# Optimization experiments

Hardware: AMD Instinct MI355X
Metric: run time of the kernel (lower is better)

The kernel has to match this reference:

```python
import jax, jax.numpy as jnp
import numpy as np

B, Hd, Wd, C, NH, WS = 8, 128, 128, 192, 6, 8
HDIM = int(C * 2.0)   # FFN hidden = 384
RED = C // 8          # AIM channel-gate reduction = 24


def setup_inputs() -> dict:
    key = jax.random.key(0)
    ks = jax.random.split(key, 12)
    s = 0.02
    return {
        "x": jax.random.normal(ks[0], (B, Hd * Wd, C), jnp.float32),
        "H": Hd,
        "W": Wd,
        "n1_w": jnp.ones((C,), jnp.float32),
        "n1_b": jnp.zeros((C,), jnp.float32),
        "qkv_w": jax.random.normal(ks[1], (C, 3 * C), jnp.float32) * s,
        "proj_w": jax.random.normal(ks[2], (C, C), jnp.float32) * s,
        "proj_b": jnp.zeros((C,), jnp.float32),
        "attn_bias": jax.random.normal(ks[3], (NH, WS * WS, WS * WS), jnp.float32) * s,
        "conv_w": jax.random.normal(ks[4], (C, 1, 3, 3), jnp.float32) * s,
        "cg_w1": jax.random.normal(ks[5], (RED, C), jnp.float32) * s,
        "cg_w2": jax.random.normal(ks[6], (C, RED), jnp.float32) * s,
        "n2_w": jnp.ones((C,), jnp.float32),
        "n2_b": jnp.zeros((C,), jnp.float32),
        "fc1_w": jax.random.normal(ks[7], (C, HDIM), jnp.float32) * s,
        "smix_w": jax.random.normal(ks[8], (HDIM, 1, 3, 3), jnp.float32) * s,
        "fc2_w": jax.random.normal(ks[9], (HDIM, C), jnp.float32) * s,
    }


def _ln(x, w, b):
    m = x.mean(-1, keepdims=True)
    v = ((x - m) ** 2).mean(-1, keepdims=True)
    return (x - m) * jax.lax.rsqrt(v + 1e-5) * w + b


def _dwconv(x, w, H, W):
    # x: [B, L, Cx] -> depthwise 3x3 'same' conv -> [B, L, Cx]
    Bx, L, Cx = x.shape
    xi = x.transpose(0, 2, 1).reshape(Bx, Cx, H, W)
    y = jax.lax.conv_general_dilated(
        xi, w, (1, 1), 'SAME', feature_group_count=Cx,
        dimension_numbers=('NCHW', 'OIHW', 'NCHW'))
    return y.reshape(Bx, Cx, L).transpose(0, 2, 1)


def _window_attn(x, H, W, qkv_w, proj_w, proj_b, bias):
    Bx, L, Cx = x.shape
    nHw, nWw = H // WS, W // WS  # H, W are multiples of WS here (no padding needed)
    hd = Cx // NH
    # [B, L, C] -> [B*nH*nW, ws*ws, C]
    xw = (x.reshape(Bx, nHw, WS, nWw, WS, Cx)
           .transpose(0, 1, 3, 2, 4, 5)
           .reshape(Bx * nHw * nWw, WS * WS, Cx))
    qkv = (xw @ qkv_w).reshape(-1, WS * WS, 3, NH, hd).transpose(2, 0, 3, 1, 4)
    q, k, v = qkv[0], qkv[1], qkv[2]          # [Bw, nh, N, hd]
    logits = (q * hd ** -0.5) @ k.transpose(0, 1, 3, 2) + bias[None]
    attn = jax.nn.softmax(logits, axis=-1)
    out = (attn @ v).transpose(0, 2, 1, 3).reshape(-1, WS * WS, Cx)
    out = out @ proj_w + proj_b
    # windows -> [B, L, C]
    return (out.reshape(Bx, nHw, nWw, WS, WS, Cx)
               .transpose(0, 1, 3, 2, 4, 5)
               .reshape(Bx, L, Cx))


def reference(x, H, W, n1_w, n1_b, qkv_w, proj_w, proj_b, attn_bias,
              conv_w, cg_w1, cg_w2, n2_w, n2_b, fc1_w, smix_w, fc2_w):
    n1 = _ln(x, n1_w, n1_b)
    attn_feat = _window_attn(n1, H, W, qkv_w, proj_w, proj_b, attn_bias)
    conv_feat = jax.nn.gelu(_dwconv(n1, conv_w, H, W), approximate=False)
    # AIM: channel_modulates_spatial (btype == 'spatial')
    pooled = conv_feat.mean(axis=1)                                   # [B, C]
    cm = jax.nn.sigmoid(jax.nn.gelu(pooled @ cg_w1.T, approximate=False) @ cg_w2.T)
    x = x + attn_feat * cm[:, None, :] + conv_feat                    # residual (DropPath=id)
    # FFN with depthwise spatial mixing
    n2 = _ln(x, n2_w, n2_b)
    h = jax.nn.gelu(n2 @ fc1_w, approximate=False)                    # [B, L, HDIM]
    h = _dwconv(h, smix_w, H, W)
    return x + h @ fc2_w
```

## Files before the change

### kernel.cpp

```cpp
#include <hip/hip_runtime.h>
#include <hip/hip_bf16.h>
#include <math.h>

#define BATCH 8
#define CCH 192
#define LTOK 16384
#define BL 131072LL
#define NWIN 2048
#define NHEADS 6

typedef __hip_bfloat16 bf16;
typedef __bf16 bfr;
typedef bfr bf16x8 __attribute__((ext_vector_type(8)));
typedef float f32x4 __attribute__((ext_vector_type(4)));
typedef unsigned short u16x8 __attribute__((ext_vector_type(8)));
typedef unsigned short u16x4 __attribute__((ext_vector_type(4)));
typedef unsigned int u32x2 __attribute__((ext_vector_type(2)));

#define FX     0
#define FN1W   1
#define FN1B   2
#define FQKVW  3
#define FPROJW 4
#define FPROJB 5
#define FBIAS  6
#define FCONVW 7
#define FCG1   8
#define FCG2   9
#define FN2W   10
#define FN2B   11
#define FFC1   12
#define FSMIX  13
#define FFC2   14

struct InPtrs { const void* p[15]; int n[15]; };

__device__ __forceinline__ float ldin(const void* p, long long i, int f32) {
    return f32 ? ((const float*)p)[i]
               : __bfloat162float(((const bf16*)p)[i]);
}

__device__ __forceinline__ float bfcvt(unsigned short u) {
    return __uint_as_float((unsigned)u << 16);
}

__device__ __forceinline__ f32x4 ld4f(const void* p, long long i, int f32) {
    if (f32) return *(const f32x4*)((const float*)p + i);
    u16x4 v = *(const u16x4*)((const bf16*)p + i);
    f32x4 r;
    r[0] = bfcvt(v[0]); r[1] = bfcvt(v[1]); r[2] = bfcvt(v[2]); r[3] = bfcvt(v[3]);
    return r;
}
__device__ __forceinline__ f32x4 ld4b(const bf16* p, long long i) {
    u16x4 v = *(const u16x4*)(p + i);
    f32x4 r;
    r[0] = bfcvt(v[0]); r[1] = bfcvt(v[1]); r[2] = bfcvt(v[2]); r[3] = bfcvt(v[3]);
    return r;
}
__device__ __forceinline__ void st4b(bf16* p, long long i, f32x4 v) {
    union { bf16 h; unsigned short u; } cv;
    u16x4 o;
    cv.h = __float2bfloat16(v[0]); o[0] = cv.u;
    cv.h = __float2bfloat16(v[1]); o[1] = cv.u;
    cv.h = __float2bfloat16(v[2]); o[2] = cv.u;
    cv.h = __float2bfloat16(v[3]); o[3] = cv.u;
    *(u16x4*)(p + i) = o;
}

__device__ __forceinline__ unsigned pk2bf(float a, float b) {
    union { bf16 h; unsigned short u; } ca, cb;
    ca.h = __float2bfloat16(a);
    cb.h = __float2bfloat16(b);
    return (unsigned)ca.u | ((unsigned)cb.u << 16);
}

__device__ __forceinline__ float gelu_f(float v) {
    return 0.5f * v * (1.0f + erff(v * 0.70710678118654752f));
}

__global__ void probe_k(InPtrs in, int* flags) {
    __shared__ int s_insane, s_evennz, s_oddnz;
    if (threadIdx.x == 0) { s_insane = 0; s_evennz = 0; s_oddnz = 0; }
    __syncthreads();
    int t = blockIdx.x;
    const bf16* p = (const bf16*)in.p[t];
    int n = in.n[t];
    int m = n < 2048 ? n : 2048;
    bool insane = false, evennz = false, oddnz = false;
    for (int i = threadIdx.x; i < m; i += 256) {
        float v = __bfloat162float(p[i]);
        if (!(fabsf(v) <= 1e9f)) insane = true;
        if (v != 0.0f) { if (i & 1) oddnz = true; else evennz = true; }
    }
    if (insane) s_insane = 1;
    if (evennz) s_evennz = 1;
    if (oddnz)  s_oddnz = 1;
    __syncthreads();
    if (threadIdx.x == 0)
        flags[t] = (s_insane || (!s_evennz && s_oddnz)) ? 1 : 0;
}

__global__ void transpose_k(const void* __restrict__ W, bf16* __restrict__ WT,
                            int K, int N, const int* flag) {
    int f = *flag;
    int idx = blockIdx.x * 256 + threadIdx.x;
    if (idx >= K * N) return;
    int k = idx / N, n = idx % N;
    WT[(long long)n * K + k] = __float2bfloat16(ldin(W, idx, f));
}

__global__ void convw_k(const void* __restrict__ W, float* __restrict__ WT,
                        int CX, const int* flag) {
    int f = *flag;
    int idx = blockIdx.x * 256 + threadIdx.x;
    if (idx >= CX * 9) return;
    int c = idx / 9, t = idx - c * 9;
    WT[t * CX + c] = ldin(W, idx, f);
}

__global__ __launch_bounds__(256)
void ln_kernel(const void* __restrict__ x, const void* __restrict__ w,
               const void* __restrict__ b, bf16* __restrict__ out,
               const int* flags) {
    int fx = flags[FX], fw = flags[FN1W], fb = flags[FN1B];
    int wv = threadIdx.x >> 6, lane = threadIdx.x & 63;
    int gw = lane >> 4, l16 = lane & 15;
    long long t = (long long)blockIdx.x * 16 + wv * 4 + gw;
    long long base = t * CCH;
    f32x4 v[3];
#pragma unroll
    for (int k = 0; k < 3; ++k)
        v[k] = ld4f(x, base + l16 * 4 + 64 * k, fx);
    float s = 0.f;
#pragma unroll
    for (int k = 0; k < 3; ++k) s += v[k][0] + v[k][1] + v[k][2] + v[k][3];
    s += __shfl_xor(s, 1); s += __shfl_xor(s, 2);
    s += __shfl_xor(s, 4); s += __shfl_xor(s, 8);
    float mean = s * (1.0f / 192.0f);
    float vs = 0.f;
#pragma unroll
    for (int k = 0; k < 3; ++k)
#pragma unroll
        for (int j = 0; j < 4; ++j) {
            float d = v[k][j] - mean;
            vs += d * d;
        }
    vs += __shfl_xor(vs, 1); vs += __shfl_xor(vs, 2);
    vs += __shfl_xor(vs, 4); vs += __shfl_xor(vs, 8);
    float rstd = rsqrtf(vs * (1.0f / 192.0f) + 1e-5f);
#pragma unroll
    for (int k = 0; k < 3; ++k) {
        int c0 = l16 * 4 + 64 * k;
        f32x4 wv4 = ld4f(w, c0, fw);
        f32x4 bv4 = ld4f(b, c0, fb);
        f32x4 o;
#pragma unroll
        for (int j = 0; j < 4; ++j)
            o[j] = (v[k][j] - mean) * rstd * wv4[j] + bv4[j];
        st4b(out, base + c0, o);
    }
}

template<int EPI, int KK, int NN, typename CT>
__global__ __launch_bounds__(256)
void gemm2_k(const bf16* __restrict__ A_, const bf16* __restrict__ BT_,
             CT* __restrict__ Cmat, const void* __restrict__ bias,
             const float* __restrict__ res, const int* __restrict__ flags) {
    constexpr int KT = KK / 192;
    constexpr int NC = NN / 64;
    constexpr int NITER = NC * KT;
    constexpr int GSTR = KK * 2;
    __shared__ __align__(16) char Ts[64 * 384];

    const int fb = (EPI == 1) ? flags[FPROJB] : 0;
    const int tid = threadIdx.x;
    const int lane = tid & 63, wv = tid >> 6;
    const int r16 = lane & 15, q = lane >> 4;
    const long long m0 = (long long)blockIdx.x * 64;
    const int swz = (r16 & 7) << 4;

    f32x4 pre[6];
    auto loadB = [&](int itn) {
        int nc2 = itn / KT, kt2 = itn - nc2 * KT;
#pragma unroll
        for (int p = 0; p < 6; ++p) {
            int off = p * 4096 + tid * 16;
            int row = off / 384, col = off - row * 384;
            pre[p] = *(const f32x4*)((const char*)BT_ +
                     (long long)(nc2 * 64 + row) * GSTR + kt2 * 384 + col);
        }
    };
    auto writeT = [&]() {
#pragma unroll
        for (int p = 0; p < 6; ++p) {
            int off = p * 4096 + tid * 16;
            int row = off / 384, col = off - row * 384;
            *(f32x4*)(Ts + row * 384 + (col ^ ((row & 7) << 4))) = pre[p];
        }
    };

    loadB(0);

    bf16x8 afrag[KK / 32];
    const char* Arow = Ts + (wv * 16 + r16) * 384;
    const char* asrc = (const char*)(A_ + m0 * KK);
#pragma unroll
    for (int kt = 0; kt < KT; ++kt) {
#pragma unroll
        for (int p = 0; p < 6; ++p) {
            int off = p * 4096 + tid * 16;
            int row = off / 384, col = off - row * 384;
            *(f32x4*)(Ts + row * 384 + (col ^ ((row & 7) << 4))) =
                *(const f32x4*)(asrc + (long long)row * GSTR + kt * 384 + col);
        }
        __syncthreads();
#pragma unroll
        for (int ks = 0; ks < 6; ++ks)
            afrag[kt * 6 + ks] = *(const bf16x8*)(Arow + ((ks * 64 + q * 16) ^ swz));
        __syncthreads();
    }
    writeT();
    __syncthreads();

    f32x4 acc0, acc1, acc2, acc3;
    float resv[16];

    for (int it = 0; it < NITER; ++it) {
        const int nc = it / KT, kt = it - nc * KT;
        if (kt == 0) {
            acc0 = f32x4{0.f, 0.f, 0.f, 0.f};
            acc1 = acc0; acc2 = acc0; acc3 = acc0;
            if (EPI == 3) {
#pragma unroll
                for (int j = 0; j < 4; ++j)
#pragma unroll
                    for (int r = 0; r < 4; ++r)
                        resv[j * 4 + r] =
                            res[(m0 + wv * 16 + q * 4 + r) * NN + nc * 64 + j * 16 + r16];
            }
        }
        const bool nxt = (it + 1 < NITER);
        if (nxt) loadB(it + 1);
#pragma unroll
        for (int ks = 0; ks < 6; ++ks) {
            bf16x8 a = afrag[kt * 6 + ks];
            const char* bb = Ts + r16 * 384 + ((ks * 64 + q * 16) ^ swz);
            bf16x8 b0 = *(const bf16x8*)(bb);
            bf16x8 b1 = *(const bf16x8*)(bb + 16 * 384);
            bf16x8 b2 = *(const bf16x8*)(bb + 32 * 384);
            bf16x8 b3 = *(const bf16x8*)(bb + 48 * 384);
            acc0 = __builtin_amdgcn_mfma_f32_16x16x32_bf16(a, b0, acc0, 0, 0, 0);
            acc1 = __builtin_amdgcn_mfma_f32_16x16x32_bf16(a, b1, acc1, 0, 0, 0);
            acc2 = __builtin_amdgcn_mfma_f32_16x16x32_bf16(a, b2, acc2, 0, 0, 0);
            acc3 = __builtin_amdgcn_mfma_f32_16x16x32_bf16(a, b3, acc3, 0, 0, 0);
        }
        __syncthreads();
        if (nxt) writeT();
        if (kt == KT - 1) {
            f32x4 accs[4] = {acc0, acc1, acc2, acc3};
#pragma unroll
            for (int j = 0; j < 4; ++j) {
                int col = nc * 64 + j * 16 + r16;
#pragma unroll
                for (int r = 0; r < 4; ++r) {
                    long long row = m0 + wv * 16 + q * 4 + r;
                    float v = accs[j][r];
                    if (EPI == 1) v += ldin(bias, col, fb);
                    if (EPI == 2) v = gelu_f(v);
                    if (EPI == 3) v += resv[j * 4 + r];
                    Cmat[row * NN + col] = (CT)v;
                }
            }
        }
        if (nxt) __syncthreads();
    }
}

__global__ __launch_bounds__(384)
void attn_proj_k(const bf16* __restrict__ qkv, const void* __restrict__ bias,
                 const bf16* __restrict__ pwT, const void* __restrict__ proj_b,
                 bf16* __restrict__ attnf, const int* __restrict__ flags) {
    __shared__ __align__(16) char SM[24576];

    const int fbias = flags[FBIAS];
    const int h = threadIdx.x >> 6, lane = threadIdx.x & 63;
    const int w = blockIdx.x;
    const int b = w >> 8, rem = w & 255, wy = rem >> 4, wx = rem & 15;
    const int l15 = lane & 15, quad = lane >> 4;
    const long long tokbase = (long long)b * LTOK + (wy * 8) * 128 + wx * 8;
    bfr* vtp = (bfr*)(SM + h * 4096);

    long long vt = tokbase + (lane >> 3) * 128 + (lane & 7);
    const bfr* vp = (const bfr*)(qkv + vt * 576 + 384 + h * 32);
    bf16x8 v0 = *(const bf16x8*)(vp);
    bf16x8 v1 = *(const bf16x8*)(vp + 8);
    bf16x8 v2 = *(const bf16x8*)(vp + 16);
    bf16x8 v3 = *(const bf16x8*)(vp + 24);

    bf16x8 aq[4], bk[4];
#pragma unroll
    for (int mt = 0; mt < 4; ++mt) {
        int i0 = mt * 16 + l15;
        long long t = tokbase + (i0 >> 3) * 128 + (i0 & 7);
        const bfr* qp = (const bfr*)(qkv + t * 576 + h * 32 + quad * 8);
        aq[mt] = *(const bf16x8*)qp;
        bk[mt] = *(const bf16x8*)(qp + 192);
    }

#pragma unroll
    for (int j = 0; j < 8; ++j) {
        int sc = lane ^ (j << 3);
        vtp[j * 64 + sc]        = v0[j];
        vtp[(j + 8) * 64 + sc]  = v1[j];
        vtp[(j + 16) * 64 + sc] = v2[j];
        vtp[(j + 24) * 64 + sc] = v3[j];
    }

    f32x4 T[4][4];
#pragma unroll
    for (int ti = 0; ti < 4; ++ti)
#pragma unroll
        for (int tj = 0; tj < 4; ++tj) {
            f32x4 z = {0.f, 0.f, 0.f, 0.f};
            T[ti][tj] = __builtin_amdgcn_mfma_f32_16x16x32_bf16(bk[ti], aq[tj], z, 0, 0, 0);
        }

    const float scale = 0.17677669529663689f;
    const long long bias0 = (long long)h * 4096;
    unsigned Wreg[4][4][2];
#pragma unroll
    for (int tj = 0; tj < 4; ++tj) {
        const long long brow = bias0 + (tj * 16 + l15) * 64 + quad * 4;
        float mloc = -3.0e38f;
#pragma unroll
        for (int ti = 0; ti < 4; ++ti) {
            f32x4 bv4 = ld4f(bias, brow + ti * 16, fbias);
#pragma unroll
            for (int r = 0; r < 4; ++r) {
                float v = T[ti][tj][r] * scale + bv4[r];
                T[ti][tj][r] = v;
                mloc = fmaxf(mloc, v);
            }
        }
        mloc = fmaxf(mloc, __shfl_xor(mloc, 16));
        mloc = fmaxf(mloc, __shfl_xor(mloc, 32));
        float l = 0.f;
#pragma unroll
        for (int ti = 0; ti < 4; ++ti)
#pragma unroll
            for (int r = 0; r < 4; ++r) {
                float e = __expf(T[ti][tj][r] - mloc);
                T[ti][tj][r] = e;
                l += e;
            }
        l += __shfl_xor(l, 16);
        l += __shfl_xor(l, 32);
        float linv = 1.0f / l;
#pragma unroll
        for (int ti = 0; ti < 4; ++ti) {
            Wreg[tj][ti][0] = pk2bf(T[ti][tj][0] * linv, T[ti][tj][1] * linv);
            Wreg[tj][ti][1] = pk2bf(T[ti][tj][2] * linv, T[ti][tj][3] * linv);
        }
    }

    const int vsw = (l15 & 7) << 3;
    bf16x8 bv[2][2];
#pragma unroll
    for (int kc = 0; kc < 2; ++kc) {
        bv[kc][0] = *(const bf16x8*)&vtp[l15 * 64 + ((kc * 32 + quad * 8) ^ vsw)];
        bv[kc][1] = *(const bf16x8*)&vtp[(16 + l15) * 64 + ((kc * 32 + quad * 8) ^ vsw)];
    }
    const int hi = quad >> 1, qlow = quad & 1;
    f32x4 O[4][2];
#pragma unroll
    for (int tj = 0; tj < 4; ++tj) {
        O[tj][0] = f32x4{0.f, 0.f, 0.f, 0.f};
        O[tj][1] = O[tj][0];
    }
#pragma unroll
    for (int tj = 0; tj < 4; ++tj)
#pragma unroll
        for (int kc = 0; kc < 2; ++kc) {
            union { unsigned u[4]; bf16x8 v; } ap;
#pragma unroll
            for (int j2 = 0; j2 < 4; ++j2) {
                int srcl = (2 * qlow + (j2 >> 1)) * 16 + l15;
                unsigned va = (unsigned)__shfl((int)Wreg[tj][2 * kc][j2 & 1], srcl);
                unsigned vb = (unsigned)__shfl((int)Wreg[tj][2 * kc + 1][j2 & 1], srcl);
                ap.u[j2] = hi ? vb : va;
            }
            O[tj][0] = __builtin_amdgcn_mfma_f32_16x16x32_bf16(ap.v, bv[kc][0], O[tj][0], 0, 0, 0);
            O[tj][1] = __builtin_amdgcn_mfma_f32_16x16x32_bf16(ap.v, bv[kc][1], O[tj][1], 0, 0, 0);
        }

    __syncthreads();

#pragma unroll
    for (int tj = 0; tj < 4; ++tj)
#pragma unroll
        for (int n2 = 0; n2 < 2; ++n2)
#pragma unroll
            for (int r = 0; r < 4; ++r) {
                int row = tj * 16 + quad * 4 + r;
                int cb = (h * 64 + n2 * 32 + l15 * 2) ^ ((row & 7) << 4);
                *(bf16*)(SM + row * 384 + cb) = __float2bfloat16(O[tj][n2][r]);
            }

    __syncthreads();

    const int fpb = flags[FPROJB];
    const int csw = (l15 & 7) << 4;
    f32x4 pacc[4][2];
#pragma unroll
    for (int mt = 0; mt < 4; ++mt) {
        pacc[mt][0] = f32x4{0.f, 0.f, 0.f, 0.f};
        pacc[mt][1] = pacc[mt][0];
    }
#pragma unroll
    for (int ks = 0; ks < 6; ++ks) {
        bf16x8 af[4];
#pragma unroll
        for (int mt = 0; mt < 4; ++mt)
            af[mt] = *(const bf16x8*)(SM + (mt * 16 + l15) * 384 +
                                      ((ks * 64 + quad * 16) ^ csw));
#pragma unroll
        for (int nt = 0; nt < 2; ++nt) {
            int col = h * 32 + nt * 16 + l15;
            bf16x8 bw = *(const bf16x8*)((const bfr*)pwT + (long long)col * 192 + ks * 32 + quad * 8);
#pragma unroll
            for (int mt = 0; mt < 4; ++mt)
                pacc[mt][nt] = __builtin_amdgcn_mfma_f32_16x16x32_bf16(af[mt], bw, pacc[mt][nt], 0, 0, 0);
        }
    }

#pragma unroll
    for (int nt = 0; nt < 2; ++nt) {
        int col = h * 32 + nt * 16 + l15;
        float bv2 = ldin(proj_b, col, fpb);
#pragma unroll
        for (int mt = 0; mt < 4; ++mt)
#pragma unroll
            for (int r = 0; r < 4; ++r) {
                long long row = (long long)w * 64 + mt * 16 + quad * 4 + r;
                attnf[row * CCH + col] = __float2bfloat16(pacc[mt][nt][r] + bv2);
            }
    }
}

template<bool GELU, int CX>
__global__ __launch_bounds__(256)
void dwconv_s4_k(const bf16* __restrict__ in, const float* __restrict__ wt,
                 bf16* __restrict__ out) {
    constexpr int CG = CX / 8;
    int cpx = gridDim.x >> 3;
    int lb = (blockIdx.x & 7) * cpx + (blockIdx.x >> 3);
    long long idx = (long long)lb * 256 + threadIdx.x;
    if (idx >= (BL / 4) * CG) return;
    int cg = (int)(idx % CG);
    long long s = idx / CG;
    int xs = (int)(s & 31);
    long long by = s >> 5;
    int y = (int)(by & 127);
    int x0 = xs * 4;
    int c0 = cg * 8;
    const long long rowpix = by * 128;

    float acc[4][8] = {};
#pragma unroll
    for (int dy = -1; dy <= 1; ++dy) {
        int yy = y + dy;
        if (yy < 0 || yy > 127) continue;
        const bf16* rp = in + ((rowpix + dy * 128) + x0) * CX + c0;
        float fcol[6][8];
#pragma unroll
        for (int ci = 0; ci < 6; ++ci) {
            int xx = x0 + ci - 1;
            if (xx < 0 || xx > 127) {
#pragma unroll
                for (int j = 0; j < 8; ++j) fcol[ci][j] = 0.f;
            } else {
                u16x8 v = *(const u16x8*)(rp + (ci - 1) * CX);
#pragma unroll
                for (int j = 0; j < 8; ++j) fcol[ci][j] = bfcvt(v[j]);
            }
        }
        const float* wb = wt + (dy + 1) * 3 * CX + c0;
#pragma unroll
        for (int dx = 0; dx < 3; ++dx) {
            f32x4 w0 = *(const f32x4*)(wb + dx * CX);
            f32x4 w1 = *(const f32x4*)(wb + dx * CX + 4);
#pragma unroll
            for (int px = 0; px < 4; ++px) {
#pragma unroll
                for (int j = 0; j < 4; ++j) {
                    acc[px][j]     += fcol[px + dx][j]     * w0[j];
                    acc[px][j + 4] += fcol[px + dx][j + 4] * w1[j];
                }
            }
        }
    }
#pragma unroll
    for (int px = 0; px < 4; ++px) {
        __attribute__((aligned(16))) unsigned short ob[8];
#pragma unroll
        for (int j = 0; j < 8; ++j) {
            float vv = acc[px][j];
            if (GELU) vv = gelu_f(vv);
            union { bf16 h; unsigned short u; } cv;
            cv.h = __float2bfloat16(vv);
            ob[j] = cv.u;
        }
        *(u16x8*)(out + (rowpix + x0 + px) * CX + c0) = *(const u16x8*)ob;
    }
}

__global__ __launch_bounds__(192)
void pool_k(const bf16* __restrict__ conv, float* __restrict__ pooled) {
    __shared__ float red[8][192];
    int b = blockIdx.x, chunk = blockIdx.y;
    int cg = threadIdx.x % 24, rr = threadIdx.x / 24;
    float acc[8] = {0.f, 0.f, 0.f, 0.f, 0.f, 0.f, 0.f, 0.f};
    long long rowbase = (long long)b * LTOK + chunk * 256;
    for (int r = rr; r < 256; r += 8) {
        u16x8 v = *(const u16x8*)(conv + (rowbase + r) * CCH + cg * 8);
#pragma unroll
        for (int j = 0; j < 8; ++j) acc[j] += bfcvt(v[j]);
    }
#pragma unroll
    for (int j = 0; j < 8; ++j) red[rr][cg * 8 + j] = acc[j];
    __syncthreads();
    if (rr == 0) {
#pragma unroll
        for (int j = 0; j < 8; ++j) {
            float s = 0.f;
#pragma unroll
            for (int i = 0; i < 8; ++i) s += red[i][cg * 8 + j];
            atomicAdd(&pooled[b * CCH + cg * 8 + j], s);
        }
    }
}

__global__ void cm_k(const float* __restrict__ pooled, const void* __restrict__ w1,
                     const void* __restrict__ w2, float* __restrict__ cm,
                     const int* flags) {
    __shared__ float ps[192], g[24];
    int f1 = flags[FCG1], f2 = flags[FCG2];
    int b = blockIdx.x, c = threadIdx.x;
    ps[c] = pooled[b * CCH + c] * (1.0f / 16384.0f);
    __syncthreads();
    if (c < 24) {
        float t = 0.f;
        for (int k = 0; k < 192; ++k) t += ps[k] * ldin(w1, c * 192 + k, f1);
        g[c] = gelu_f(t);
    }
    __syncthreads();
    float s = 0.f;
#pragma unroll
    for (int r = 0; r < 24; ++r) s += g[r] * ldin(w2, c * 24 + r, f2);
    cm[b * CCH + c] = 1.0f / (1.0f + expf(-s));
}

__global__ __launch_bounds__(256)
void x2ln2_k(const void* __restrict__ x, const bf16* __restrict__ attnf,
             const bf16* __restrict__ conv, const float* __restrict__ cm,
             const void* __restrict__ w, const void* __restrict__ bb,
             float* __restrict__ x2, bf16* __restrict__ n2, const int* flags) {
    int fx = flags[FX], fw = flags[FN2W], fb = flags[FN2B];
    int wv = threadIdx.x >> 6, lane = threadIdx.x & 63;
    int gw = lane >> 4, l16 = lane & 15;
    long long t = (long long)blockIdx.x * 16 + wv * 4 + gw;
    int b = (int)(t >> 14);
    int l = (int)(t & 16383);
    int y = l >> 7, xx = l & 127;
    long long wrow = ((long long)b * 256 + (y >> 3) * 16 + (xx >> 3)) * 64 + (y & 7) * 8 + (xx & 7);

    f32x4 sv[3];
#pragma unroll
    for (int k = 0; k < 3; ++k) {
        int c0 = l16 * 4 + 64 * k;
        f32x4 xv  = ld4f(x, t * CCH + c0, fx);
        f32x4 af  = ld4b(attnf, wrow * CCH + c0);
        f32x4 cf  = ld4b(conv, t * CCH + c0);
        f32x4 cmv = *(const f32x4*)(cm + b * CCH + c0);
        f32x4 o;
#pragma unroll
        for (int j = 0; j < 4; ++j)
            o[j] = xv[j] + af[j] * cmv[j] + cf[j];
        *(f32x4*)(x2 + t * CCH + c0) = o;
        sv[k] = o;
    }
    float s = 0.f;
#pragma unroll
    for (int k = 0; k < 3; ++k) s += sv[k][0] + sv[k][1] + sv[k][2] + sv[k][3];
    s += __shfl_xor(s, 1); s += __shfl_xor(s, 2);
    s += __shfl_xor(s, 4); s += __shfl_xor(s, 8);
    float mean = s * (1.0f / 192.0f);
    float vs = 0.f;
#pragma unroll
    for (int k = 0; k < 3; ++k)
#pragma unroll
        for (int j = 0; j < 4; ++j) {
            float d = sv[k][j] - mean;
            vs += d * d;
        }
    vs += __shfl_xor(vs, 1); vs += __shfl_xor(vs, 2);
    vs += __shfl_xor(vs, 4); vs += __shfl_xor(vs, 8);
    float rstd = rsqrtf(vs * (1.0f / 192.0f) + 1e-5f);
#pragma unroll
    for (int k = 0; k < 3; ++k) {
        int c0 = l16 * 4 + 64 * k;
        f32x4 wv4 = ld4f(w, c0, fw);
        f32x4 bv4 = ld4f(bb, c0, fb);
        f32x4 o;
#pragma unroll
        for (int j = 0; j < 4; ++j)
            o[j] = (sv[k][j] - mean) * rstd * wv4[j] + bv4[j];
        st4b(n2, t * CCH + c0, o);
    }
}

extern "C" void kernel_launch(void* const* d_in, const int* in_sizes, int n_in,
                              void* d_out, int out_size, void* d_ws, size_t ws_size,
                              hipStream_t stream) {
    (void)n_in; (void)out_size; (void)ws_size;
    float* out = (float*)d_out;

    char* wsp = (char*)d_ws;
    size_t off = 0;
    auto alloc = [&](size_t bytes) -> char* {
        char* p = wsp + off;
        off += (bytes + 255) & ~(size_t)255;
        return p;
    };
    int*  flags   = (int*)alloc(15 * 4);
    bf16* qkv_wT  = (bf16*)alloc(576 * 192 * 2);
    bf16* proj_wT = (bf16*)alloc(192 * 192 * 2);
    bf16* fc1_wT  = (bf16*)alloc(384 * 192 * 2);
    bf16* fc2_wT  = (bf16*)alloc(192 * 384 * 2);
    float* convwT = (float*)alloc(9 * CCH * 4);
    float* smixwT = (float*)alloc(9 * 384 * 4);
    float* pooled = (float*)alloc(BATCH * CCH * 4);
    float* cm     = (float*)alloc(BATCH * CCH * 4);
    char* Rbig    = alloc(BL * 576 * 2);
    char* Rpair   = alloc(BL * 384 * 2);

    bf16* qkvb  = (bf16*)Rbig;
    bf16* convf = (bf16*)Rbig;
    bf16* hbuf  = (bf16*)Rbig;
    bf16* n1    = (bf16*)Rpair;
    bf16* attnf = (bf16*)(Rpair + (size_t)BL * 192 * 2);
    bf16* n2    = n1;
    bf16* h2    = (bf16*)Rpair;
    float* x2   = out;

    const int imap[15] = {0, 3, 4, 5, 6, 7, 8, 9, 10, 11, 12, 13, 14, 15, 16};
    InPtrs ip;
    for (int i = 0; i < 15; ++i) { ip.p[i] = d_in[imap[i]]; ip.n[i] = in_sizes[imap[i]]; }
    const void* x        = d_in[0];
    const void* qkv_w    = d_in[5];
    const void* proj_w   = d_in[6];
    const void* proj_b   = d_in[7];
    const void* attnbias = d_in[8];
    const void* conv_w   = d_in[9];
    const void* cg_w1    = d_in[10];
    const void* cg_w2    = d_in[11];
    const void* fc1_w    = d_in[14];
    const void* smix_w   = d_in[15];
    const void* fc2_w    = d_in[16];

    probe_k<<<15, 256, 0, stream>>>(ip, flags);

    transpose_k<<<(192 * 576 + 255) / 256, 256, 0, stream>>>(qkv_w, qkv_wT, 192, 576, flags + FQKVW);
    transpose_k<<<(192 * 192 + 255) / 256, 256, 0, stream>>>(proj_w, proj_wT, 192, 192, flags + FPROJW);
    transpose_k<<<(192 * 384 + 255) / 256, 256, 0, stream>>>(fc1_w, fc1_wT, 192, 384, flags + FFC1);
    transpose_k<<<(384 * 192 + 255) / 256, 256, 0, stream>>>(fc2_w, fc2_wT, 384, 192, flags + FFC2);
    convw_k<<<(CCH * 9 + 255) / 256, 256, 0, stream>>>(conv_w, convwT, CCH, flags + FCONVW);
    convw_k<<<(384 * 9 + 255) / 256, 256, 0, stream>>>(smix_w, smixwT, 384, flags + FSMIX);
    hipMemsetAsync(pooled, 0, BATCH * CCH * 4, stream);

    ln_kernel<<<BL / 16, 256, 0, stream>>>(x, d_in[3], d_in[4], n1, flags);
    gemm2_k<0, 192, 576, bf16><<<BL / 64, 256, 0, stream>>>(n1, qkv_wT, qkvb, nullptr, nullptr, flags);
    attn_proj_k<<<NWIN, 384, 0, stream>>>(qkvb, attnbias, proj_wT, proj_b, attnf, flags);
    dwconv_s4_k<true, 192><<<(int)(BL / 4 * 24 / 256), 256, 0, stream>>>(n1, convwT, convf);
    pool_k<<<dim3(BATCH, 64), 192, 0, stream>>>(convf, pooled);
    cm_k<<<BATCH, 192, 0, stream>>>(pooled, cg_w1, cg_w2, cm, flags);
    x2ln2_k<<<BL / 16, 256, 0, stream>>>(x, attnf, convf, cm, d_in[12], d_in[13], x2, n2, flags);
    gemm2_k<2, 192, 384, bf16><<<BL / 64, 256, 0, stream>>>(n2, fc1_wT, hbuf, nullptr, nullptr, flags);
    dwconv_s4_k<false, 384><<<(int)(BL / 4 * 48 / 256), 256, 0, stream>>>(hbuf, smixwT, h2);
    gemm2_k<3, 384, 192, float><<<BL / 64, 256, 0, stream>>>(h2, fc2_wT, out, nullptr, x2, flags);
}
```

Baseline: 612.6 us.

## Scatter QKV GEMM output into per-window per-head layout and prefetch proj weights

The QKV GEMM epilogue (EPI==0) now writes q, k and v into a [sel][window][head][token][dim] layout, so the attention kernel reads contiguous 4 KB chunks per head instead of strided token rows. The attention kernel also loads the projection weights and bias into registers before the barrier so their global latency overlaps with the shared-memory writes. In exchange, the GEMM stores become scattered scalar writes with extra index arithmetic, and the prefetched weights raise register pressure.

```diff
diff --git a/kernel.cpp b/kernel.cpp
--- a/kernel.cpp
+++ b/kernel.cpp
@@ -268,7 +268,17 @@
                     if (EPI == 1) v += ldin(bias, col, fb);
                     if (EPI == 2) v = gelu_f(v);
                     if (EPI == 3) v += resv[j * 4 + r];
-                    Cmat[row * NN + col] = (CT)v;
+                    if (EPI == 0) {
+                        int bb2 = (int)(row >> 14), l = (int)(row & 16383);
+                        int y = l >> 7, xx = l & 127;
+                        long long ww = (long long)bb2 * 256 + (y >> 3) * 16 + (xx >> 3);
+                        int tin = (y & 7) * 8 + (xx & 7);
+                        int sel = col / 192, rem = col - sel * 192;
+                        int hh = rem >> 5, d = rem & 31;
+                        Cmat[((((long long)sel * NWIN + ww) * 6 + hh) * 64 + tin) * 32 + d] = (CT)v;
+                    } else {
+                        Cmat[row * NN + col] = (CT)v;
+                    }
                 }
             }
         }
@@ -277,7 +287,7 @@
 }
 
 __global__ __launch_bounds__(384)
-void attn_proj_k(const bf16* __restrict__ qkv, const void* __restrict__ bias,
+void attn_proj_k(const bf16* __restrict__ qkvw, const void* __restrict__ bias,
                  const bf16* __restrict__ pwT, const void* __restrict__ proj_b,
                  bf16* __restrict__ attnf, const int* __restrict__ flags) {
     __shared__ __align__(16) char SM[24576];
@@ -285,13 +295,14 @@
     const int fbias = flags[FBIAS];
     const int h = threadIdx.x >> 6, lane = threadIdx.x & 63;
     const int w = blockIdx.x;
-    const int b = w >> 8, rem = w & 255, wy = rem >> 4, wx = rem & 15;
     const int l15 = lane & 15, quad = lane >> 4;
-    const long long tokbase = (long long)b * LTOK + (wy * 8) * 128 + wx * 8;
     bfr* vtp = (bfr*)(SM + h * 4096);
 
-    long long vt = tokbase + (lane >> 3) * 128 + (lane & 7);
-    const bfr* vp = (const bfr*)(qkv + vt * 576 + 384 + h * 32);
+    const bfr* qb = (const bfr*)qkvw + ((long long)w * 6 + h) * 2048;
+    const bfr* kb = qb + (long long)NWIN * 6 * 2048;
+    const bfr* vb = kb + (long long)NWIN * 6 * 2048;
+
+    const bfr* vp = vb + lane * 32;
     bf16x8 v0 = *(const bf16x8*)(vp);
     bf16x8 v1 = *(const bf16x8*)(vp + 8);
     bf16x8 v2 = *(const bf16x8*)(vp + 16);
@@ -300,11 +311,9 @@
     bf16x8 aq[4], bk[4];
 #pragma unroll
     for (int mt = 0; mt < 4; ++mt) {
-        int i0 = mt * 16 + l15;
-        long long t = tokbase + (i0 >> 3) * 128 + (i0 & 7);
-        const bfr* qp = (const bfr*)(qkv + t * 576 + h * 32 + quad * 8);
-        aq[mt] = *(const bf16x8*)qp;
-        bk[mt] = *(const bf16x8*)(qp + 192);
+        int off = (mt * 16 + l15) * 32 + quad * 8;
+        aq[mt] = *(const bf16x8*)(qb + off);
+        bk[mt] = *(const bf16x8*)(kb + off);
     }
 
 #pragma unroll
@@ -386,12 +395,24 @@
             for (int j2 = 0; j2 < 4; ++j2) {
                 int srcl = (2 * qlow + (j2 >> 1)) * 16 + l15;
                 unsigned va = (unsigned)__shfl((int)Wreg[tj][2 * kc][j2 & 1], srcl);
-                unsigned vb = (unsigned)__shfl((int)Wreg[tj][2 * kc + 1][j2 & 1], srcl);
-                ap.u[j2] = hi ? vb : va;
+                unsigned vb2 = (unsigned)__shfl((int)Wreg[tj][2 * kc + 1][j2 & 1], srcl);
+                ap.u[j2] = hi ? vb2 : va;
             }
             O[tj][0] = __builtin_amdgcn_mfma_f32_16x16x32_bf16(ap.v, bv[kc][0], O[tj][0], 0, 0, 0);
             O[tj][1] = __builtin_amdgcn_mfma_f32_16x16x32_bf16(ap.v, bv[kc][1], O[tj][1], 0, 0, 0);
         }
+
+    const int fpb = flags[FPROJB];
+    bf16x8 pw[2][6];
+    float pbv[2];
+#pragma unroll
+    for (int nt = 0; nt < 2; ++nt) {
+        int col = h * 32 + nt * 16 + l15;
+        pbv[nt] = ldin(proj_b, col, fpb);
+#pragma unroll
+        for (int ks = 0; ks < 6; ++ks)
+            pw[nt][ks] = *(const bf16x8*)((const bfr*)pwT + (long long)col * 192 + ks * 32 + quad * 8);
+    }
 
     __syncthreads();
 
@@ -408,7 +429,6 @@
 
     __syncthreads();
 
-    const int fpb = flags[FPROJB];
     const int csw = (l15 & 7) << 4;
     f32x4 pacc[4][2];
 #pragma unroll
@@ -424,25 +444,21 @@
             af[mt] = *(const bf16x8*)(SM + (mt * 16 + l15) * 384 +
                                       ((ks * 64 + quad * 16) ^ csw));
 #pragma unroll
-        for (int nt = 0; nt < 2; ++nt) {
-            int col = h * 32 + nt * 16 + l15;
-            bf16x8 bw = *(const bf16x8*)((const bfr*)pwT + (long long)col * 192 + ks * 32 + quad * 8);
+        for (int nt = 0; nt < 2; ++nt)
 #pragma unroll
             for (int mt = 0; mt < 4; ++mt)
-                pacc[mt][nt] = __builtin_amdgcn_mfma_f32_16x16x32_bf16(af[mt], bw, pacc[mt][nt], 0, 0, 0);
-        }
+                pacc[mt][nt] = __builtin_amdgcn_mfma_f32_16x16x32_bf16(af[mt], pw[nt][ks], pacc[mt][nt], 0, 0, 0);
     }
 
 #pragma unroll
     for (int nt = 0; nt < 2; ++nt) {
         int col = h * 32 + nt * 16 + l15;
-        float bv2 = ldin(proj_b, col, fpb);
 #pragma unroll
         for (int mt = 0; mt < 4; ++mt)
 #pragma unroll
             for (int r = 0; r < 4; ++r) {
                 long long row = (long long)w * 64 + mt * 16 + quad * 4 + r;
-                attnf[row * CCH + col] = __float2bfloat16(pacc[mt][nt][r] + bv2);
+                attnf[row * CCH + col] = __float2bfloat16(pacc[mt][nt][r] + pbv[nt]);
             }
     }
 }
```

After: 616.1 us. Within noise of the previous version (+0.6%).
